# Kernel tuning notes

Measured on AMD Instinct MI355X. Metric: run time of the kernel, lower is better.

The kernel has to match this reference:

```python
import jax, jax.numpy as jnp
import numpy as np

HIDDEN = 256

def setup_inputs() -> dict:
    key = jax.random.key(0)
    k1, k2, k3, k4, k5 = jax.random.split(key, 5)
    hidden = jax.random.normal(k1, (1, 32, HIDDEN), dtype=jnp.float32)
    encoder_outputs = jax.random.normal(k2, (32, 8192, HIDDEN), dtype=jnp.float32)
    # nn.Linear(hidden*2, hidden): weight (H, 2H), bias (H,)
    W = jax.random.normal(k3, (HIDDEN, 2 * HIDDEN), dtype=jnp.float32) / np.sqrt(2 * HIDDEN)
    b = jax.random.normal(k4, (HIDDEN,), dtype=jnp.float32) * 0.01
    v = jax.random.uniform(k5, (HIDDEN,), dtype=jnp.float32)
    return {"hidden": hidden, "encoder_outputs": encoder_outputs, "W": W, "b": b, "v": v}

def reference(hidden, encoder_outputs, W, b, v):
    # hidden: (1, B, H) -> (B, 1, H); avoid materializing the concat by
    # splitting Linear(2H->H) into two matmuls (same math as cat + Linear).
    Wh, We = W[:, :HIDDEN], W[:, HIDDEN:]          # each (H, 2H/2)
    h = jnp.transpose(hidden, (1, 0, 2))           # (B, 1, H)
    # (B,1,H)@(H,H)^T broadcasts over seq; (B,S,H)@(H,H)^T
    pre = jnp.einsum('boh,kh->bok', h, Wh) + jnp.einsum('bsh,kh->bsk', encoder_outputs, We) + b
    scores = jnp.tanh(pre)                          # (B, S, H)
    logits = jnp.einsum('bsh,h->bs', scores, v)     # (B, S)
    attn_weights = jax.nn.softmax(logits, axis=1)   # (B, S)
    context = jnp.einsum('bs,bsh->bh', attn_weights, encoder_outputs)  # (B, H)
    return (context, attn_weights)
```

## Files before the change

### kernel.cpp

```cpp
#include <hip/hip_runtime.h>


typedef _Float16 f16x8 __attribute__((ext_vector_type(8)));
typedef _Float16 f16x4 __attribute__((ext_vector_type(4)));
typedef float    f32x4 __attribute__((ext_vector_type(4)));

__device__ __forceinline__ float fast_tanh(float x){
  x = fminf(15.f, fmaxf(-15.f, x));
  float e = __expf(2.f * x);
  return (e - 1.f) * __builtin_amdgcn_rcpf(e + 1.f);
}

__global__ void prep_kernel(const float* __restrict__ hidden, const float* __restrict__ W,
                            const float* __restrict__ bias, _Float16* __restrict__ Bfrag,
                            float* __restrict__ qb)
{
  int blk = blockIdx.x;
  if (blk < 256){
    int tid  = blk * 256 + threadIdx.x;
    int j    = tid & 7;
    int lane = (tid >> 3) & 63;
    int kc   = (tid >> 9) & 7;
    int nt   = tid >> 12;
    int lc   = lane & 15, q = lane >> 4;
    int row  = nt * 16 + lc;
    int col  = 256 + kc * 32 + q * 8 + j;
    Bfrag[tid] = (_Float16)W[row * 512 + col];
  } else {
    int b = blk - 256;
    int k = threadIdx.x;
    const float4* hp = (const float4*)(hidden + b * 256);
    const float4* wp = (const float4*)(W + k * 512);
    float s = 0.f;
    for (int i = 0; i < 64; i++){
      float4 h4 = hp[i], w4 = wp[i];
      s += h4.x * w4.x + h4.y * w4.y + h4.z * w4.z + h4.w * w4.w;
    }
    qb[b * 256 + k] = s + bias[k];
  }
}

__global__ __launch_bounds__(512) void attn_main(
    const float* __restrict__ enc, const _Float16* __restrict__ Bfrag,
    const float* __restrict__ qb, const float* __restrict__ v,
    float* __restrict__ logits, float* __restrict__ P,
    float* __restrict__ mw, float* __restrict__ lw)
{
  __shared__ _Float16 Af[16384];
  __shared__ float plg[8][64];
  __shared__ float sw[64];
  __shared__ float Pl2[2][256];

  const int b = blockIdx.x >> 7, chunk = blockIdx.x & 127;
  const int tid = threadIdx.x, wv = tid >> 6, lane = tid & 63;
  const int q = lane >> 4, lc = lane & 15;
  const int rowBase = b * 8192 + chunk * 64;

  const int nt0 = wv * 2;
  f16x8 Breg[2][8];
  {
    const f16x8* Bsrc = (const f16x8*)Bfrag;
    #pragma unroll
    for (int ntl = 0; ntl < 2; ntl++)
      #pragma unroll
      for (int kc = 0; kc < 8; kc++)
        Breg[ntl][kc] = Bsrc[((nt0 + ntl) * 8 + kc) * 64 + lane];
  }
  float qv[2], vv[2];
  #pragma unroll
  for (int ntl = 0; ntl < 2; ntl++){
    int col = (nt0 + ntl) * 16 + lc;
    qv[ntl] = qb[b * 256 + col];
    vv[ntl] = v[col];
  }

  {
    const int r = tid >> 3, kc = tid & 7;
    const float4* src = (const float4*)(enc + (size_t)(rowBase + r) * 256 + kc * 32);
    const int mt = r >> 4, lcr = r & 15;
    #pragma unroll
    for (int i = 0; i < 8; i++){
      float4 x = src[i];
      f16x4 h4;
      h4[0] = (_Float16)x.x; h4[1] = (_Float16)x.y;
      h4[2] = (_Float16)x.z; h4[3] = (_Float16)x.w;
      int idx = (((mt * 8 + kc) * 64 + (i >> 1) * 16 + lcr) * 8 + (i & 1) * 4);
      *(f16x4*)(&Af[idx]) = h4;
    }
  }
  __syncthreads();

  {
    const f16x8* Afp = (const f16x8*)Af;
    #pragma unroll
    for (int mt = 0; mt < 4; mt++){
      f32x4 acc0 = {0, 0, 0, 0}, acc1 = {0, 0, 0, 0};
      #pragma unroll
      for (int kc = 0; kc < 8; kc++){
        f16x8 af = Afp[(mt * 8 + kc) * 64 + lane];
        acc0 = __builtin_amdgcn_mfma_f32_16x16x32_f16(af, Breg[0][kc], acc0, 0, 0, 0);
        acc1 = __builtin_amdgcn_mfma_f32_16x16x32_f16(af, Breg[1][kc], acc1, 0, 0, 0);
      }
      #pragma unroll
      for (int r = 0; r < 4; r++){
        float s = fast_tanh(acc0[r] + qv[0]) * vv[0] + fast_tanh(acc1[r] + qv[1]) * vv[1];
        s += __shfl_xor(s, 1); s += __shfl_xor(s, 2);
        s += __shfl_xor(s, 4); s += __shfl_xor(s, 8);
        if (lc == 0) plg[wv][mt * 16 + q * 4 + r] = s;
      }
    }
  }
  __syncthreads();

  if (tid < 64){
    float x = 0.f;
    #pragma unroll
    for (int w = 0; w < 8; w++) x += plg[w][tid];
    logits[rowBase + tid] = x;
    float m = x;
    for (int o = 1; o < 64; o <<= 1) m = fmaxf(m, __shfl_xor(m, o));
    float e = __expf(x - m);
    sw[tid] = e;
    float s2 = e;
    for (int o = 1; o < 64; o <<= 1) s2 += __shfl_xor(s2, o);
    if (tid == 0){ mw[blockIdx.x] = m; lw[blockIdx.x] = s2; }
  }
  __syncthreads();

  {
    const int k = tid & 255, h = tid >> 8;
    const float* ep = enc + (size_t)(rowBase + h * 32) * 256 + k;
    const float* swh = sw + h * 32;
    float s0 = 0.f, s1 = 0.f, s2 = 0.f, s3 = 0.f;
    #pragma unroll
    for (int r4 = 0; r4 < 8; r4++){
      s0 += swh[r4 * 4 + 0] * ep[(size_t)(r4 * 4 + 0) * 256];
      s1 += swh[r4 * 4 + 1] * ep[(size_t)(r4 * 4 + 1) * 256];
      s2 += swh[r4 * 4 + 2] * ep[(size_t)(r4 * 4 + 2) * 256];
      s3 += swh[r4 * 4 + 3] * ep[(size_t)(r4 * 4 + 3) * 256];
    }
    Pl2[h][k] = (s0 + s1) + (s2 + s3);
  }
  __syncthreads();
  if (tid < 256) P[(size_t)blockIdx.x * 256 + tid] = Pl2[0][tid] + Pl2[1][tid];
}

__global__ void attn_finish(const float* __restrict__ logits, const float* __restrict__ P,
                            const float* __restrict__ mw, const float* __restrict__ lw,
                            float* __restrict__ out)
{
  const int b = blockIdx.x, t = threadIdx.x;
  __shared__ float sm[128], sw[128], se[128], sM[1], sL[1];
  if (t < 128){ sm[t] = mw[b * 128 + t]; sw[t] = lw[b * 128 + t]; }
  __syncthreads();
  if (t == 0){
    float M = -1e30f;
    for (int i = 0; i < 128; i++) M = fmaxf(M, sm[i]);
    sM[0] = M;
  }
  __syncthreads();
  const float M = sM[0];
  if (t < 128) se[t] = __expf(sm[t] - M);
  __syncthreads();
  if (t == 0){
    float L = 0.f;
    for (int i = 0; i < 128; i++) L += sw[i] * se[i];
    sL[0] = L;
  }
  __syncthreads();
  const float inv = 1.f / sL[0];
  float c = 0.f;
  for (int ch = 0; ch < 128; ch++) c += se[ch] * P[(size_t)(b * 128 + ch) * 256 + t];
  out[b * 256 + t] = c * inv;
  const float* lg = logits + (size_t)b * 8192;
  float* ao = out + 8192 + (size_t)b * 8192;
  for (int s = t; s < 8192; s += 256) ao[s] = __expf(lg[s] - M) * inv;
}

extern "C" void kernel_launch(void* const* d_in, const int* in_sizes, int n_in,
                              void* d_out, int out_size, void* d_ws, size_t ws_size,
                              hipStream_t stream)
{
  const float* hidden = (const float*)d_in[0];
  const float* enc    = (const float*)d_in[1];
  const float* W      = (const float*)d_in[2];
  const float* bias   = (const float*)d_in[3];
  const float* v      = (const float*)d_in[4];
  float* out = (float*)d_out;

  char* ws = (char*)d_ws;
  _Float16* Bfrag = (_Float16*)ws;
  float* qb     = (float*)(ws + (128 << 10));
  float* logits = (float*)(ws + (160 << 10));
  float* P      = (float*)(ws + (160 << 10) + (1 << 20));
  float* mw     = (float*)(ws + (160 << 10) + (5 << 20));
  float* lw     = (float*)(ws + (160 << 10) + (5 << 20) + (16 << 10));

  prep_kernel<<<288, 256, 0, stream>>>(hidden, W, bias, Bfrag, qb);
  attn_main<<<4096, 512, 0, stream>>>(enc, Bfrag, qb, v, logits, P, mw, lw);
  attn_finish<<<32, 256, 0, stream>>>(logits, P, mw, lw, out);
}
```

Measured before the change: 413.1 us.

## Make attention blocks persistent over four chunks with register prefetch of next tile

```diff
diff --git a/kernel.cpp b/kernel.cpp
--- a/kernel.cpp
+++ b/kernel.cpp
@@ -40,7 +40,7 @@
   }
 }
 
-__global__ __launch_bounds__(512) void attn_main(
+__global__ __launch_bounds__(512, 2) void attn_main(
     const float* __restrict__ enc, const _Float16* __restrict__ Bfrag,
     const float* __restrict__ qb, const float* __restrict__ v,
     float* __restrict__ logits, float* __restrict__ P,
@@ -51,10 +51,9 @@
   __shared__ float sw[64];
   __shared__ float Pl2[2][256];
 
-  const int b = blockIdx.x >> 7, chunk = blockIdx.x & 127;
+  const int b = blockIdx.x >> 5, grp = blockIdx.x & 31;
   const int tid = threadIdx.x, wv = tid >> 6, lane = tid & 63;
   const int q = lane >> 4, lc = lane & 15;
-  const int rowBase = b * 8192 + chunk * 64;
 
   const int nt0 = wv * 2;
   f16x8 Breg[2][8];
@@ -63,8 +62,8 @@
     #pragma unroll
     for (int ntl = 0; ntl < 2; ntl++)
       #pragma unroll
-      for (int kc = 0; kc < 8; kc++)
-        Breg[ntl][kc] = Bsrc[((nt0 + ntl) * 8 + kc) * 64 + lane];
+      for (int kc2 = 0; kc2 < 8; kc2++)
+        Breg[ntl][kc2] = Bsrc[((nt0 + ntl) * 8 + kc2) * 64 + lane];
   }
   float qv[2], vv[2];
   #pragma unroll
@@ -74,107 +73,136 @@
     vv[ntl] = v[col];
   }
 
+  const int sr = tid >> 3, skc = tid & 7;
+  const int smt = sr >> 4, slcr = sr & 15;
+
+  float4 pf[8];
+
   {
-    const int r = tid >> 3, kc = tid & 7;
-    const float4* src = (const float4*)(enc + (size_t)(rowBase + r) * 256 + kc * 32);
-    const int mt = r >> 4, lcr = r & 15;
+    const float4* src = (const float4*)(enc + (size_t)(b * 8192 + grp * 256 + sr) * 256 + skc * 32);
+    #pragma unroll
+    for (int i = 0; i < 8; i++) pf[i] = src[i];
     #pragma unroll
     for (int i = 0; i < 8; i++){
-      float4 x = src[i];
       f16x4 h4;
-      h4[0] = (_Float16)x.x; h4[1] = (_Float16)x.y;
-      h4[2] = (_Float16)x.z; h4[3] = (_Float16)x.w;
-      int idx = (((mt * 8 + kc) * 64 + (i >> 1) * 16 + lcr) * 8 + (i & 1) * 4);
+      h4[0] = (_Float16)pf[i].x; h4[1] = (_Float16)pf[i].y;
+      h4[2] = (_Float16)pf[i].z; h4[3] = (_Float16)pf[i].w;
+      int idx = (((smt * 8 + skc) * 64 + (i >> 1) * 16 + slcr) * 8 + (i & 1) * 4);
       *(f16x4*)(&Af[idx]) = h4;
     }
   }
   __syncthreads();
 
-  {
-    const f16x8* Afp = (const f16x8*)Af;
-    #pragma unroll
-    for (int mt = 0; mt < 4; mt++){
-      f32x4 acc0 = {0, 0, 0, 0}, acc1 = {0, 0, 0, 0};
-      #pragma unroll
-      for (int kc = 0; kc < 8; kc++){
-        f16x8 af = Afp[(mt * 8 + kc) * 64 + lane];
-        acc0 = __builtin_amdgcn_mfma_f32_16x16x32_f16(af, Breg[0][kc], acc0, 0, 0, 0);
-        acc1 = __builtin_amdgcn_mfma_f32_16x16x32_f16(af, Breg[1][kc], acc1, 0, 0, 0);
+  for (int c = 0; c < 4; c++){
+    const int chunk = grp * 4 + c;
+    const int rowBase = b * 8192 + chunk * 64;
+
+    if (c < 3){
+      const float4* src = (const float4*)(enc + (size_t)(rowBase + 64 + sr) * 256 + skc * 32);
+      #pragma unroll
+      for (int i = 0; i < 8; i++) pf[i] = src[i];
+    }
+
+    {
+      const f16x8* Afp = (const f16x8*)Af;
+      #pragma unroll
+      for (int m = 0; m < 4; m++){
+        f32x4 acc0 = {0, 0, 0, 0}, acc1 = {0, 0, 0, 0};
+        #pragma unroll
+        for (int k8 = 0; k8 < 8; k8++){
+          f16x8 af = Afp[(m * 8 + k8) * 64 + lane];
+          acc0 = __builtin_amdgcn_mfma_f32_16x16x32_f16(af, Breg[0][k8], acc0, 0, 0, 0);
+          acc1 = __builtin_amdgcn_mfma_f32_16x16x32_f16(af, Breg[1][k8], acc1, 0, 0, 0);
+        }
+        #pragma unroll
+        for (int rr = 0; rr < 4; rr++){
+          float s = fast_tanh(acc0[rr] + qv[0]) * vv[0] + fast_tanh(acc1[rr] + qv[1]) * vv[1];
+          s += __shfl_xor(s, 1); s += __shfl_xor(s, 2);
+          s += __shfl_xor(s, 4); s += __shfl_xor(s, 8);
+          if (lc == 0) plg[wv][m * 16 + q * 4 + rr] = s;
+        }
       }
-      #pragma unroll
-      for (int r = 0; r < 4; r++){
-        float s = fast_tanh(acc0[r] + qv[0]) * vv[0] + fast_tanh(acc1[r] + qv[1]) * vv[1];
-        s += __shfl_xor(s, 1); s += __shfl_xor(s, 2);
-        s += __shfl_xor(s, 4); s += __shfl_xor(s, 8);
-        if (lc == 0) plg[wv][mt * 16 + q * 4 + r] = s;
+    }
+    __syncthreads();
+
+    if (tid < 64){
+      float x = 0.f;
+      #pragma unroll
+      for (int w = 0; w < 8; w++) x += plg[w][tid];
+      logits[rowBase + tid] = x;
+      float mx = x;
+      for (int o = 1; o < 64; o <<= 1) mx = fmaxf(mx, __shfl_xor(mx, o));
+      float e = __expf(x - mx);
+      sw[tid] = e;
+      float s2 = e;
+      for (int o = 1; o < 64; o <<= 1) s2 += __shfl_xor(s2, o);
+      if (tid == 0){ mw[b * 128 + chunk] = mx; lw[b * 128 + chunk] = s2; }
+    }
+    if (c < 3){
+      #pragma unroll
+      for (int i = 0; i < 8; i++){
+        f16x4 h4;
+        h4[0] = (_Float16)pf[i].x; h4[1] = (_Float16)pf[i].y;
+        h4[2] = (_Float16)pf[i].z; h4[3] = (_Float16)pf[i].w;
+        int idx = (((smt * 8 + skc) * 64 + (i >> 1) * 16 + slcr) * 8 + (i & 1) * 4);
+        *(f16x4*)(&Af[idx]) = h4;
       }
     }
-  }
-  __syncthreads();
-
-  if (tid < 64){
-    float x = 0.f;
-    #pragma unroll
-    for (int w = 0; w < 8; w++) x += plg[w][tid];
-    logits[rowBase + tid] = x;
-    float m = x;
-    for (int o = 1; o < 64; o <<= 1) m = fmaxf(m, __shfl_xor(m, o));
-    float e = __expf(x - m);
-    sw[tid] = e;
-    float s2 = e;
-    for (int o = 1; o < 64; o <<= 1) s2 += __shfl_xor(s2, o);
-    if (tid == 0){ mw[blockIdx.x] = m; lw[blockIdx.x] = s2; }
-  }
-  __syncthreads();
-
-  {
-    const int k = tid & 255, h = tid >> 8;
-    const float* ep = enc + (size_t)(rowBase + h * 32) * 256 + k;
-    const float* swh = sw + h * 32;
-    float s0 = 0.f, s1 = 0.f, s2 = 0.f, s3 = 0.f;
-    #pragma unroll
-    for (int r4 = 0; r4 < 8; r4++){
-      s0 += swh[r4 * 4 + 0] * ep[(size_t)(r4 * 4 + 0) * 256];
-      s1 += swh[r4 * 4 + 1] * ep[(size_t)(r4 * 4 + 1) * 256];
-      s2 += swh[r4 * 4 + 2] * ep[(size_t)(r4 * 4 + 2) * 256];
-      s3 += swh[r4 * 4 + 3] * ep[(size_t)(r4 * 4 + 3) * 256];
-    }
-    Pl2[h][k] = (s0 + s1) + (s2 + s3);
-  }
-  __syncthreads();
-  if (tid < 256) P[(size_t)blockIdx.x * 256 + tid] = Pl2[0][tid] + Pl2[1][tid];
+    __syncthreads();
+
+    {
+      const int k = tid & 255, h = tid >> 8;
+      const float* ep = enc + (size_t)(rowBase + h * 32) * 256 + k;
+      const float* swh = sw + h * 32;
+      float s0 = 0.f, s1 = 0.f, s2 = 0.f, s3 = 0.f;
+      #pragma unroll
+      for (int r4 = 0; r4 < 8; r4++){
+        s0 += swh[r4 * 4 + 0] * ep[(size_t)(r4 * 4 + 0) * 256];
+        s1 += swh[r4 * 4 + 1] * ep[(size_t)(r4 * 4 + 1) * 256];
+        s2 += swh[r4 * 4 + 2] * ep[(size_t)(r4 * 4 + 2) * 256];
+        s3 += swh[r4 * 4 + 3] * ep[(size_t)(r4 * 4 + 3) * 256];
+      }
+      Pl2[h][k] = (s0 + s1) + (s2 + s3);
+    }
+    __syncthreads();
+    if (tid < 256) P[(size_t)(b * 128 + chunk) * 256 + tid] = Pl2[0][tid] + Pl2[1][tid];
+  }
 }
 
 __global__ void attn_finish(const float* __restrict__ logits, const float* __restrict__ P,
                             const float* __restrict__ mw, const float* __restrict__ lw,
                             float* __restrict__ out)
 {
-  const int b = blockIdx.x, t = threadIdx.x;
-  __shared__ float sm[128], sw[128], se[128], sM[1], sL[1];
-  if (t < 128){ sm[t] = mw[b * 128 + t]; sw[t] = lw[b * 128 + t]; }
+  const int b = blockIdx.x >> 1, half = blockIdx.x & 1, t = threadIdx.x;
+  __shared__ float sm[128], swl[128], se[128], sML[2];
+  if (t < 128){ sm[t] = mw[b * 128 + t]; swl[t] = lw[b * 128 + t]; }
   __syncthreads();
   if (t == 0){
     float M = -1e30f;
     for (int i = 0; i < 128; i++) M = fmaxf(M, sm[i]);
-    sM[0] = M;
-  }
-  __syncthreads();
-  const float M = sM[0];
+    sML[0] = M;
+  }
+  __syncthreads();
+  const float M = sML[0];
   if (t < 128) se[t] = __expf(sm[t] - M);
   __syncthreads();
   if (t == 0){
     float L = 0.f;
-    for (int i = 0; i < 128; i++) L += sw[i] * se[i];
-    sL[0] = L;
-  }
-  __syncthreads();
-  const float inv = 1.f / sL[0];
-  float c = 0.f;
-  for (int ch = 0; ch < 128; ch++) c += se[ch] * P[(size_t)(b * 128 + ch) * 256 + t];
-  out[b * 256 + t] = c * inv;
-  const float* lg = logits + (size_t)b * 8192;
-  float* ao = out + 8192 + (size_t)b * 8192;
-  for (int s = t; s < 8192; s += 256) ao[s] = __expf(lg[s] - M) * inv;
+    for (int i = 0; i < 128; i++) L += swl[i] * se[i];
+    sML[1] = L;
+  }
+  __syncthreads();
+  const float inv = 1.f / sML[1];
+  if (half == 0){
+    float c = 0.f;
+    #pragma unroll 8
+    for (int ch = 0; ch < 128; ch++) c += se[ch] * P[(size_t)(b * 128 + ch) * 256 + t];
+    out[b * 256 + t] = c * inv;
+  }
+  const float* lg = logits + (size_t)b * 8192 + half * 4096;
+  float* ao = out + 8192 + (size_t)b * 8192 + half * 4096;
+  #pragma unroll
+  for (int s2 = 0; s2 < 16; s2++) ao[s2 * 256 + t] = __expf(lg[s2 * 256 + t] - M) * inv;
 }
 
 extern "C" void kernel_launch(void* const* d_in, const int* in_sizes, int n_in,
@@ -197,6 +225,6 @@
   float* lw     = (float*)(ws + (160 << 10) + (5 << 20) + (16 << 10));
 
   prep_kernel<<<288, 256, 0, stream>>>(hidden, W, bias, Bfrag, qb);
-  attn_main<<<4096, 512, 0, stream>>>(enc, Bfrag, qb, v, logits, P, mw, lw);
-  attn_finish<<<32, 256, 0, stream>>>(logits, P, mw, lw, out);
-}
+  attn_main<<<1024, 512, 0, stream>>>(enc, Bfrag, qb, v, logits, P, mw, lw);
+  attn_finish<<<64, 256, 0, stream>>>(logits, P, mw, lw, out);
+}
```

Result: slower. 458.6 us (+11.0%).

## Stage full weight in LDS, per-wave 32-row chunks with register-held encoder fragments

Applied to the files above, without the earlier changes.

```diff
diff --git a/kernel.cpp b/kernel.cpp
--- a/kernel.cpp
+++ b/kernel.cpp
@@ -2,13 +2,16 @@
 
 
 typedef _Float16 f16x8 __attribute__((ext_vector_type(8)));
-typedef _Float16 f16x4 __attribute__((ext_vector_type(4)));
 typedef float    f32x4 __attribute__((ext_vector_type(4)));
 
 __device__ __forceinline__ float fast_tanh(float x){
   x = fminf(15.f, fmaxf(-15.f, x));
   float e = __expf(2.f * x);
   return (e - 1.f) * __builtin_amdgcn_rcpf(e + 1.f);
+}
+
+__device__ __forceinline__ float lane_bcast(float x, int l){
+  return __uint_as_float(__builtin_amdgcn_readlane(__float_as_uint(x), l));
 }
 
 __global__ void prep_kernel(const float* __restrict__ hidden, const float* __restrict__ W,
@@ -40,141 +43,145 @@
   }
 }
 
-__global__ __launch_bounds__(512) void attn_main(
+__global__ __launch_bounds__(1024) void attn_main(
     const float* __restrict__ enc, const _Float16* __restrict__ Bfrag,
     const float* __restrict__ qb, const float* __restrict__ v,
     float* __restrict__ logits, float* __restrict__ P,
     float* __restrict__ mw, float* __restrict__ lw)
 {
-  __shared__ _Float16 Af[16384];
-  __shared__ float plg[8][64];
-  __shared__ float sw[64];
-  __shared__ float Pl2[2][256];
-
-  const int b = blockIdx.x >> 7, chunk = blockIdx.x & 127;
+  __shared__ _Float16 Wf[65536];
+  __shared__ float2 qv2[256];
+
   const int tid = threadIdx.x, wv = tid >> 6, lane = tid & 63;
   const int q = lane >> 4, lc = lane & 15;
-  const int rowBase = b * 8192 + chunk * 64;
-
-  const int nt0 = wv * 2;
-  f16x8 Breg[2][8];
+  const int b = blockIdx.x >> 3, slab = blockIdx.x & 7;
+
   {
-    const f16x8* Bsrc = (const f16x8*)Bfrag;
+    const float4* src = (const float4*)Bfrag;
+    float4* dst = (float4*)Wf;
     #pragma unroll
-    for (int ntl = 0; ntl < 2; ntl++)
-      #pragma unroll
-      for (int kc = 0; kc < 8; kc++)
-        Breg[ntl][kc] = Bsrc[((nt0 + ntl) * 8 + kc) * 64 + lane];
-  }
-  float qv[2], vv[2];
-  #pragma unroll
-  for (int ntl = 0; ntl < 2; ntl++){
-    int col = (nt0 + ntl) * 16 + lc;
-    qv[ntl] = qb[b * 256 + col];
-    vv[ntl] = v[col];
-  }
-
-  {
-    const int r = tid >> 3, kc = tid & 7;
-    const float4* src = (const float4*)(enc + (size_t)(rowBase + r) * 256 + kc * 32);
-    const int mt = r >> 4, lcr = r & 15;
-    #pragma unroll
-    for (int i = 0; i < 8; i++){
-      float4 x = src[i];
-      f16x4 h4;
-      h4[0] = (_Float16)x.x; h4[1] = (_Float16)x.y;
-      h4[2] = (_Float16)x.z; h4[3] = (_Float16)x.w;
-      int idx = (((mt * 8 + kc) * 64 + (i >> 1) * 16 + lcr) * 8 + (i & 1) * 4);
-      *(f16x4*)(&Af[idx]) = h4;
-    }
+    for (int i = 0; i < 8; i++) dst[tid + i * 1024] = src[tid + i * 1024];
+    if (tid < 256) qv2[tid] = make_float2(qb[b * 256 + tid], v[tid]);
   }
   __syncthreads();
 
-  {
-    const f16x8* Afp = (const f16x8*)Af;
-    #pragma unroll
-    for (int mt = 0; mt < 4; mt++){
+  const f16x8* Wl = (const f16x8*)Wf;
+  const int rowBase0 = b * 8192 + (slab * 32 + wv * 2) * 32;
+
+  f16x8 bf[2][8];
+  #define LOAD_BF(base)                                                     \
+  {                                                                         \
+    const float* er0 = enc + (size_t)((base) + lc) * 256 + q * 8;           \
+    _Pragma("unroll")                                                       \
+    for (int t = 0; t < 2; t++){                                            \
+      const float* er = er0 + t * 16 * 256;                                 \
+      _Pragma("unroll")                                                     \
+      for (int kc = 0; kc < 8; kc++){                                       \
+        float4 x0 = *(const float4*)(er + kc * 32);                         \
+        float4 x1 = *(const float4*)(er + kc * 32 + 4);                     \
+        f16x8 h;                                                            \
+        h[0]=(_Float16)x0.x; h[1]=(_Float16)x0.y;                           \
+        h[2]=(_Float16)x0.z; h[3]=(_Float16)x0.w;                           \
+        h[4]=(_Float16)x1.x; h[5]=(_Float16)x1.y;                           \
+        h[6]=(_Float16)x1.z; h[7]=(_Float16)x1.w;                           \
+        bf[t][kc] = h;                                                      \
+      }                                                                     \
+    }                                                                       \
+  }
+
+  LOAD_BF(rowBase0)
+
+  for (int ci = 0; ci < 2; ci++){
+    const int rowBase = rowBase0 + ci * 32;
+    const int cid = b * 256 + slab * 32 + wv * 2 + ci;
+
+    float lg0 = 0.f, lg1 = 0.f;
+    #pragma unroll 2
+    for (int nt = 0; nt < 16; nt++){
       f32x4 acc0 = {0, 0, 0, 0}, acc1 = {0, 0, 0, 0};
       #pragma unroll
       for (int kc = 0; kc < 8; kc++){
-        f16x8 af = Afp[(mt * 8 + kc) * 64 + lane];
-        acc0 = __builtin_amdgcn_mfma_f32_16x16x32_f16(af, Breg[0][kc], acc0, 0, 0, 0);
-        acc1 = __builtin_amdgcn_mfma_f32_16x16x32_f16(af, Breg[1][kc], acc1, 0, 0, 0);
+        f16x8 a = Wl[(nt * 8 + kc) * 64 + lane];
+        acc0 = __builtin_amdgcn_mfma_f32_16x16x32_f16(a, bf[0][kc], acc0, 0, 0, 0);
+        acc1 = __builtin_amdgcn_mfma_f32_16x16x32_f16(a, bf[1][kc], acc1, 0, 0, 0);
       }
       #pragma unroll
-      for (int r = 0; r < 4; r++){
-        float s = fast_tanh(acc0[r] + qv[0]) * vv[0] + fast_tanh(acc1[r] + qv[1]) * vv[1];
-        s += __shfl_xor(s, 1); s += __shfl_xor(s, 2);
-        s += __shfl_xor(s, 4); s += __shfl_xor(s, 8);
-        if (lc == 0) plg[wv][mt * 16 + q * 4 + r] = s;
+      for (int rr = 0; rr < 4; rr++){
+        float2 c = qv2[nt * 16 + q * 4 + rr];
+        lg0 += fast_tanh(acc0[rr] + c.x) * c.y;
+        lg1 += fast_tanh(acc1[rr] + c.x) * c.y;
       }
     }
-  }
-  __syncthreads();
-
-  if (tid < 64){
-    float x = 0.f;
+    lg0 += __shfl_xor(lg0, 16); lg0 += __shfl_xor(lg0, 32);
+    lg1 += __shfl_xor(lg1, 16); lg1 += __shfl_xor(lg1, 32);
+    if (q == 0){
+      logits[rowBase + lc]      = lg0;
+      logits[rowBase + 16 + lc] = lg1;
+    }
+    float m = fmaxf(lg0, lg1);
+    m = fmaxf(m, __shfl_xor(m, 1)); m = fmaxf(m, __shfl_xor(m, 2));
+    m = fmaxf(m, __shfl_xor(m, 4)); m = fmaxf(m, __shfl_xor(m, 8));
+    float e0 = __expf(lg0 - m), e1 = __expf(lg1 - m);
+    float ls = e0 + e1;
+    ls += __shfl_xor(ls, 1); ls += __shfl_xor(ls, 2);
+    ls += __shfl_xor(ls, 4); ls += __shfl_xor(ls, 8);
+    if (lane == 0){ mw[cid] = m; lw[cid] = ls; }
+
+    if (ci == 0) LOAD_BF(rowBase0 + 32)
+
+    float4 ctx = make_float4(0.f, 0.f, 0.f, 0.f);
+    const float* ep = enc + (size_t)rowBase * 256 + lane * 4;
     #pragma unroll
-    for (int w = 0; w < 8; w++) x += plg[w][tid];
-    logits[rowBase + tid] = x;
-    float m = x;
-    for (int o = 1; o < 64; o <<= 1) m = fmaxf(m, __shfl_xor(m, o));
-    float e = __expf(x - m);
-    sw[tid] = e;
-    float s2 = e;
-    for (int o = 1; o < 64; o <<= 1) s2 += __shfl_xor(s2, o);
-    if (tid == 0){ mw[blockIdx.x] = m; lw[blockIdx.x] = s2; }
-  }
-  __syncthreads();
-
-  {
-    const int k = tid & 255, h = tid >> 8;
-    const float* ep = enc + (size_t)(rowBase + h * 32) * 256 + k;
-    const float* swh = sw + h * 32;
-    float s0 = 0.f, s1 = 0.f, s2 = 0.f, s3 = 0.f;
-    #pragma unroll
-    for (int r4 = 0; r4 < 8; r4++){
-      s0 += swh[r4 * 4 + 0] * ep[(size_t)(r4 * 4 + 0) * 256];
-      s1 += swh[r4 * 4 + 1] * ep[(size_t)(r4 * 4 + 1) * 256];
-      s2 += swh[r4 * 4 + 2] * ep[(size_t)(r4 * 4 + 2) * 256];
-      s3 += swh[r4 * 4 + 3] * ep[(size_t)(r4 * 4 + 3) * 256];
-    }
-    Pl2[h][k] = (s0 + s1) + (s2 + s3);
-  }
-  __syncthreads();
-  if (tid < 256) P[(size_t)blockIdx.x * 256 + tid] = Pl2[0][tid] + Pl2[1][tid];
+    for (int r = 0; r < 16; r++){
+      float w0 = lane_bcast(e0, r);
+      float w1 = lane_bcast(e1, r);
+      float4 a  = *(const float4*)(ep + (size_t)r * 256);
+      float4 b4 = *(const float4*)(ep + (size_t)(r + 16) * 256);
+      ctx.x += w0 * a.x + w1 * b4.x;
+      ctx.y += w0 * a.y + w1 * b4.y;
+      ctx.z += w0 * a.z + w1 * b4.z;
+      ctx.w += w0 * a.w + w1 * b4.w;
+    }
+    *(float4*)(P + (size_t)cid * 256 + lane * 4) = ctx;
+  }
+  #undef LOAD_BF
 }
 
 __global__ void attn_finish(const float* __restrict__ logits, const float* __restrict__ P,
                             const float* __restrict__ mw, const float* __restrict__ lw,
                             float* __restrict__ out)
 {
-  const int b = blockIdx.x, t = threadIdx.x;
-  __shared__ float sm[128], sw[128], se[128], sM[1], sL[1];
-  if (t < 128){ sm[t] = mw[b * 128 + t]; sw[t] = lw[b * 128 + t]; }
+  const int b = blockIdx.x >> 1, half = blockIdx.x & 1, t = threadIdx.x;
+  __shared__ float se[256], red[8];
+  float mv = mw[b * 256 + t], lv = lw[b * 256 + t];
+  float m = mv;
+  #pragma unroll
+  for (int o = 1; o < 64; o <<= 1) m = fmaxf(m, __shfl_xor(m, o));
+  if ((t & 63) == 0) red[t >> 6] = m;
   __syncthreads();
-  if (t == 0){
-    float M = -1e30f;
-    for (int i = 0; i < 128; i++) M = fmaxf(M, sm[i]);
-    sM[0] = M;
-  }
+  const float M = fmaxf(fmaxf(red[0], red[1]), fmaxf(red[2], red[3]));
+  float e = __expf(mv - M);
+  se[t] = e;
+  float l = e * lv;
+  #pragma unroll
+  for (int o = 1; o < 64; o <<= 1) l += __shfl_xor(l, o);
+  if ((t & 63) == 0) red[4 + (t >> 6)] = l;
   __syncthreads();
-  const float M = sM[0];
-  if (t < 128) se[t] = __expf(sm[t] - M);
-  __syncthreads();
-  if (t == 0){
-    float L = 0.f;
-    for (int i = 0; i < 128; i++) L += sw[i] * se[i];
-    sL[0] = L;
-  }
-  __syncthreads();
-  const float inv = 1.f / sL[0];
-  float c = 0.f;
-  for (int ch = 0; ch < 128; ch++) c += se[ch] * P[(size_t)(b * 128 + ch) * 256 + t];
-  out[b * 256 + t] = c * inv;
-  const float* lg = logits + (size_t)b * 8192;
-  float* ao = out + 8192 + (size_t)b * 8192;
-  for (int s = t; s < 8192; s += 256) ao[s] = __expf(lg[s] - M) * inv;
+  const float L = red[4] + red[5] + red[6] + red[7];
+  const float inv = 1.f / L;
+  if (half == 0){
+    float c0 = 0.f, c1 = 0.f;
+    #pragma unroll 8
+    for (int ch = 0; ch < 128; ch++){
+      c0 += se[ch]       * P[(size_t)(b * 256 + ch) * 256 + t];
+      c1 += se[ch + 128] * P[(size_t)(b * 256 + 128 + ch) * 256 + t];
+    }
+    out[b * 256 + t] = (c0 + c1) * inv;
+  }
+  const float* lg = logits + (size_t)b * 8192 + half * 4096;
+  float* ao = out + 8192 + (size_t)b * 8192 + half * 4096;
+  #pragma unroll
+  for (int s2 = 0; s2 < 16; s2++) ao[s2 * 256 + t] = __expf(lg[s2 * 256 + t] - M) * inv;
 }
 
 extern "C" void kernel_launch(void* const* d_in, const int* in_sizes, int n_in,
@@ -193,10 +200,10 @@
   float* qb     = (float*)(ws + (128 << 10));
   float* logits = (float*)(ws + (160 << 10));
   float* P      = (float*)(ws + (160 << 10) + (1 << 20));
-  float* mw     = (float*)(ws + (160 << 10) + (5 << 20));
-  float* lw     = (float*)(ws + (160 << 10) + (5 << 20) + (16 << 10));
+  float* mw     = (float*)(ws + (160 << 10) + (9 << 20));
+  float* lw     = (float*)(ws + (160 << 10) + (9 << 20) + (32 << 10));
 
   prep_kernel<<<288, 256, 0, stream>>>(hidden, W, bias, Bfrag, qb);
-  attn_main<<<4096, 512, 0, stream>>>(enc, Bfrag, qb, v, logits, P, mw, lw);
-  attn_finish<<<32, 256, 0, stream>>>(logits, P, mw, lw, out);
-}
+  attn_main<<<256, 1024, 0, stream>>>(enc, Bfrag, qb, v, logits, P, mw, lw);
+  attn_finish<<<64, 256, 0, stream>>>(logits, P, mw, lw, out);
+}
```

Result: no change. 419.1 us (+1.5%).
